# Performance work log

Measured on AMD Instinct MI355X. Metric: run time of the kernel, lower is better.

Reference implementation:

```python
import jax, jax.numpy as jnp
import numpy as np

E = 8       # num experts
T = 1024    # num tokens
H = 1024    # hidden dim
I = 1024    # intermediate dim (per gate/up half)


def setup_inputs() -> dict:
    key = jax.random.key(0)
    k1, k2, k3, k4 = jax.random.split(key, 4)
    return {
        "hidden_states": jax.random.normal(k1, (T, H), jnp.float32),
        "router_logits": jax.random.normal(k2, (T, E), jnp.float32),
        # W13 stored pre-transposed as in the module: [E, H, 2*I]
        "W13": jax.random.normal(k3, (E, H, 2 * I), jnp.float32) * 0.02,
        # W2 stored pre-transposed: [E, I, H]
        "W2": jax.random.normal(k4, (E, I, H), jnp.float32) * 0.02,
        "top_k": 2,
    }


def reference(hidden_states, router_logits, W13, W2, top_k):
    num_experts = router_logits.shape[-1]
    # --- routing: topk_softmax (softmax over all experts, then top-k) ---
    probs = jax.nn.softmax(router_logits, axis=-1)            # [T, E]
    w, idx = jax.lax.top_k(probs, top_k)                      # [T, K]
    # renormalize=True path of moe_gather
    w = w / jnp.sum(w, axis=-1, keepdims=True)
    # combine weights per expert: [T, E]
    combine = jnp.sum(jax.nn.one_hot(idx, num_experts, dtype=w.dtype) * w[..., None], axis=1)
    # --- grouped gate-up GEMM + silu_and_mul ---
    h13 = jnp.einsum('th,ehf->tef', hidden_states, W13)       # [T, E, 2I]
    gate, up = jnp.split(h13, 2, axis=-1)                     # each [T, E, I]
    act = jax.nn.silu(gate) * up                              # silu_and_mul
    # --- grouped down GEMM ---
    down = jnp.einsum('tei,eih->teh', act, W2)                # [T, E, H]
    # --- combine (moe_gather) ---
    return jnp.einsum('te,teh->th', combine, down)            # [T, H]
```

## Files before the change

kernel.cpp:

```cpp
#include <hip/hip_runtime.h>
#include <hip/hip_bf16.h>
#include <stdint.h>

#define NE    8
#define NTOK  1024
#define NH    1024
#define NI    1024
#define N13   2048
#define NPAIR 2048

typedef __attribute__((ext_vector_type(8))) short short8;
typedef __attribute__((ext_vector_type(4))) float f32x4;
typedef unsigned short u16;
typedef unsigned int   u32;

__device__ __forceinline__ u16 f2bf(float x) {
    union { float f; u32 u; } v; v.f = x;
    return (u16)((v.u + 0x7fffu + ((v.u >> 16) & 1u)) >> 16);
}

__device__ __forceinline__ void async_ld16(u16* lds, const u16* g) {
    __builtin_amdgcn_global_load_lds(
        (const __attribute__((address_space(1))) u32*)g,
        (__attribute__((address_space(3))) u32*)lds, 16, 0, 0);
}

__global__ __launch_bounds__(256) void prep_kernel(
    const float* __restrict__ logits, const float* __restrict__ X,
    int* __restrict__ counts, int* __restrict__ pair_tok,
    float* __restrict__ pair_w, u16* __restrict__ Xb)
{
    const int tid = threadIdx.x;
    if (blockIdx.x > 0) {
        const int i = (blockIdx.x - 1) * 256 + tid;
        const float4* s = (const float4*)X;
        const float4 a = s[2 * i], b = s[2 * i + 1];
        uint4 o;
        o.x = f2bf(a.x) | ((u32)f2bf(a.y) << 16);
        o.y = f2bf(a.z) | ((u32)f2bf(a.w) << 16);
        o.z = f2bf(b.x) | ((u32)f2bf(b.y) << 16);
        o.w = f2bf(b.z) | ((u32)f2bf(b.w) << 16);
        *(uint4*)(Xb + (size_t)i * 8) = o;
        return;
    }

    __shared__ int s_cnt[NE];
    __shared__ int s_base[NE];
    if (tid < NE) s_cnt[tid] = 0;
    __syncthreads();

    int eA[4][2]; int slotA[4][2]; float wA[4][2];

    #pragma unroll
    for (int i = 0; i < 4; i++) {
        const int t = tid * 4 + i;
        float l[NE];
        #pragma unroll
        for (int e = 0; e < NE; e++) l[e] = logits[t * NE + e];
        int i0 = 0;
        #pragma unroll
        for (int e = 1; e < NE; e++) if (l[e] > l[i0]) i0 = e;
        int i1 = -1;
        #pragma unroll
        for (int e = 0; e < NE; e++) {
            if (e == i0) continue;
            if (i1 < 0 || l[e] > l[i1]) i1 = e;
        }
        const float e10 = __expf(l[i1] - l[i0]);
        const float inv = 1.0f / (1.0f + e10);
        eA[i][0] = i0; eA[i][1] = i1;
        wA[i][0] = inv; wA[i][1] = e10 * inv;
        slotA[i][0] = atomicAdd(&s_cnt[i0], 1);
        slotA[i][1] = atomicAdd(&s_cnt[i1], 1);
    }
    __syncthreads();
    if (tid == 0) {
        int acc = 0;
        #pragma unroll
        for (int e = 0; e < NE; e++) { s_base[e] = acc; acc += s_cnt[e]; }
    }
    __syncthreads();
    if (tid < NE) counts[tid] = s_cnt[tid];
    #pragma unroll
    for (int i = 0; i < 4; i++) {
        const int t = tid * 4 + i;
        #pragma unroll
        for (int k = 0; k < 2; k++) {
            const int p = s_base[eA[i][k]] + slotA[i][k];
            pair_tok[p] = t;
            pair_w[p]   = wA[i][k];
        }
    }
}

__global__ __launch_bounds__(256) void cvt_w_kernel(
    const float* __restrict__ W13, u16* __restrict__ W13t,
    const float* __restrict__ W2, u16* __restrict__ W2t)
{
    __shared__ float Ts[64][65];
    const float* src; u16* dst; int K, N, bid;
    if (blockIdx.x < NE * 16 * 32) { src = W13; dst = W13t; K = NH; N = N13; bid = blockIdx.x; }
    else                           { src = W2;  dst = W2t;  K = NI; N = NH;  bid = blockIdx.x - NE * 16 * 32; }

    const int ktiles = K >> 6, ntiles = N >> 6;
    const int tpe = ktiles * ntiles;
    const int e = bid / tpe;
    const int rem = bid - e * tpe;
    const int kt = rem / ntiles, nt = rem - (rem / ntiles) * ntiles;
    const float* sb = src + ((size_t)e * K + (size_t)kt * 64) * N + nt * 64;
    const int tid = threadIdx.x;

    #pragma unroll
    for (int i = 0; i < 4; i++) {
        const int idx = tid + i * 256;
        const int r = idx >> 4, c = (idx & 15) << 2;
        const float4 v = *(const float4*)(sb + (size_t)r * N + c);
        Ts[r][c + 0] = v.x; Ts[r][c + 1] = v.y;
        Ts[r][c + 2] = v.z; Ts[r][c + 3] = v.w;
    }
    __syncthreads();
    u16* db = dst + ((size_t)e * N + (size_t)nt * 64) * K + kt * 64;
    #pragma unroll
    for (int i = 0; i < 2; i++) {
        const int u = tid + i * 256;
        const int n = u >> 3, k8 = (u & 7) << 3;
        uint4 o;
        o.x = f2bf(Ts[k8 + 0][n]) | ((u32)f2bf(Ts[k8 + 1][n]) << 16);
        o.y = f2bf(Ts[k8 + 2][n]) | ((u32)f2bf(Ts[k8 + 3][n]) << 16);
        o.z = f2bf(Ts[k8 + 4][n]) | ((u32)f2bf(Ts[k8 + 5][n]) << 16);
        o.w = f2bf(Ts[k8 + 6][n]) | ((u32)f2bf(Ts[k8 + 7][n]) << 16);
        *(uint4*)(db + (size_t)n * K + k8) = o;
    }
}

__device__ __forceinline__ bool find_tile(
    const int* __restrict__ counts, int tile, int bm, int ntn,
    int& e_o, int& mt_o, int& nt_o, int& cnt_o, int& base_o)
{
    int base = 0;
    #pragma unroll
    for (int e = 0; e < NE; e++) {
        const int cnt = counts[e];
        const int mtiles = (cnt + bm - 1) / bm;
        const int tiles = mtiles * ntn;
        if (tile < tiles) {
            e_o = e; mt_o = tile / ntn; nt_o = tile - (tile / ntn) * ntn;
            cnt_o = cnt; base_o = base; return true;
        }
        tile -= tiles; base += cnt;
    }
    return false;
}

__global__ __launch_bounds__(256) void gemm1_kernel(
    const u16* __restrict__ Xb, const u16* __restrict__ W13t,
    const int* __restrict__ counts, const int* __restrict__ pair_tok,
    u16* __restrict__ act)
{
    int e, mt, nt, cnt, base;
    if (!find_tile(counts, blockIdx.x, 128, NI / 32, e, mt, nt, cnt, base)) return;

    __shared__ u16 As[2][128 * 32];
    __shared__ u16 Bs[2][64 * 32];

    const int tid = threadIdx.x;
    const int ct  = nt * 32;

    const int m0 = tid >> 2;
    const int sw16 = (((tid & 3) ^ (m0 & 3)) << 3);
    const int t0 = pair_tok[base + min(mt * 128 + m0, cnt - 1)];
    const int t1 = pair_tok[base + min(mt * 128 + 64 + m0, cnt - 1)];
    const u16* ga0 = Xb + (size_t)t0 * NH + sw16;
    const u16* ga1 = Xb + (size_t)t1 * NH + sw16;
    const int wcol = (m0 < 32) ? (ct + m0) : (NI + ct + m0 - 32);
    const u16* gb = W13t + ((size_t)e * N13 + wcol) * 1024 + sw16;

    const int lane = tid & 63, w = tid >> 6;
    const int quad = lane >> 4, lid = lane & 15;
    const int rw = w >> 1, cw = w & 1;
    const int fsw = (quad ^ (lid & 3)) << 3;
    int aoff[4];
    #pragma unroll
    for (int mi = 0; mi < 4; mi++)
        aoff[mi] = (rw * 64 + mi * 16 + lid) * 32 + fsw;
    const int bgoff = (cw * 16 + lid) * 32 + fsw;
    const int buoff = (32 + cw * 16 + lid) * 32 + fsw;

    f32x4 accg[4] = {};
    f32x4 accu[4] = {};

#define ISSUE1(b, k0)                                        \
    {                                                        \
        async_ld16(&As[b][tid * 8],         ga0 + (k0));     \
        async_ld16(&As[b][(tid + 256) * 8], ga1 + (k0));     \
        async_ld16(&Bs[b][tid * 8],         gb  + (k0));     \
    }
#define COMP1(b)                                                               \
    {                                                                          \
        short8 av[4];                                                          \
        _Pragma("unroll") for (int mi = 0; mi < 4; mi++)                       \
            av[mi] = *(const short8*)&As[b][aoff[mi]];                         \
        const short8 gv = *(const short8*)&Bs[b][bgoff];                       \
        const short8 uv = *(const short8*)&Bs[b][buoff];                       \
        _Pragma("unroll") for (int mi = 0; mi < 4; mi++) {                     \
            accg[mi] = __builtin_amdgcn_mfma_f32_16x16x32_bf16(                \
                av[mi], gv, accg[mi], 0, 0, 0);                                \
            accu[mi] = __builtin_amdgcn_mfma_f32_16x16x32_bf16(                \
                av[mi], uv, accu[mi], 0, 0, 0);                                \
        }                                                                      \
    }

    ISSUE1(0, 0);
    int buf = 0;
    for (int k0 = 32; k0 < NH; k0 += 32) {
        __syncthreads();
        ISSUE1(buf ^ 1, k0);
        COMP1(buf);
        buf ^= 1;
    }
    __syncthreads();
    COMP1(buf);

    const int col = ct + cw * 16 + lid;
    #pragma unroll
    for (int mi = 0; mi < 4; mi++) {
        #pragma unroll
        for (int r = 0; r < 4; r++) {
            const int row = mt * 128 + rw * 64 + mi * 16 + quad * 4 + r;
            if (row < cnt) {
                const float g = accg[mi][r], u = accu[mi][r];
                const float s = g / (1.0f + __expf(-g)) * u;
                act[(size_t)(base + row) * NI + col] = f2bf(s);
            }
        }
    }
#undef ISSUE1
#undef COMP1
}

__global__ __launch_bounds__(256) void gemm2_kernel(
    const u16* __restrict__ act, const u16* __restrict__ W2t,
    const int* __restrict__ counts, const int* __restrict__ pair_tok,
    const float* __restrict__ pair_w, float* __restrict__ out)
{
    int e, mt, nt, cnt, base;
    if (!find_tile(counts, blockIdx.x, 64, NH / 64, e, mt, nt, cnt, base)) return;

    __shared__ u16 As[2][64 * 32];
    __shared__ u16 Bs[2][64 * 32];

    const int tid = threadIdx.x;
    const int ct  = nt * 64;

    const int m0 = tid >> 2;
    const int sw16 = (((tid & 3) ^ (m0 & 3)) << 3);
    const int p0 = base + min(mt * 64 + m0, cnt - 1);
    const u16* ga = act + (size_t)p0 * NI + sw16;
    const u16* gb = W2t + ((size_t)e * 1024 + ct + m0) * 1024 + sw16;

    const int lane = tid & 63, w = tid >> 6;
    const int quad = lane >> 4, lid = lane & 15;
    const int rw = w >> 1, cw = w & 1;
    const int fsw = (quad ^ (lid & 3)) << 3;
    int aoff[2], boff[2];
    #pragma unroll
    for (int mi = 0; mi < 2; mi++)
        aoff[mi] = (rw * 32 + mi * 16 + lid) * 32 + fsw;
    #pragma unroll
    for (int nj = 0; nj < 2; nj++)
        boff[nj] = (cw * 32 + nj * 16 + lid) * 32 + fsw;

    f32x4 acc[2][2] = {};

#define ISSUE2(b, k0)                                        \
    {                                                        \
        async_ld16(&As[b][tid * 8], ga + (k0));              \
        async_ld16(&Bs[b][tid * 8], gb + (k0));              \
    }
#define COMP2(b)                                                               \
    {                                                                          \
        short8 av[2], bv[2];                                                   \
        _Pragma("unroll") for (int mi = 0; mi < 2; mi++)                       \
            av[mi] = *(const short8*)&As[b][aoff[mi]];                         \
        _Pragma("unroll") for (int nj = 0; nj < 2; nj++)                       \
            bv[nj] = *(const short8*)&Bs[b][boff[nj]];                         \
        _Pragma("unroll") for (int mi = 0; mi < 2; mi++)                       \
            _Pragma("unroll") for (int nj = 0; nj < 2; nj++)                   \
                acc[mi][nj] = __builtin_amdgcn_mfma_f32_16x16x32_bf16(         \
                    av[mi], bv[nj], acc[mi][nj], 0, 0, 0);                     \
    }

    ISSUE2(0, 0);
    int buf = 0;
    for (int k0 = 32; k0 < NI; k0 += 32) {
        __syncthreads();
        ISSUE2(buf ^ 1, k0);
        COMP2(buf);
        buf ^= 1;
    }
    __syncthreads();
    COMP2(buf);

    #pragma unroll
    for (int mi = 0; mi < 2; mi++) {
        #pragma unroll
        for (int r = 0; r < 4; r++) {
            const int row = mt * 64 + rw * 32 + mi * 16 + quad * 4 + r;
            if (row < cnt) {
                const int p = base + row;
                const int t = pair_tok[p];
                const float wgt = pair_w[p];
                #pragma unroll
                for (int nj = 0; nj < 2; nj++) {
                    const int col = ct + cw * 32 + nj * 16 + lid;
                    atomicAdd(out + (size_t)t * NH + col, wgt * acc[mi][nj][r]);
                }
            }
        }
    }
#undef ISSUE2
#undef COMP2
}

extern "C" void kernel_launch(void* const* d_in, const int* in_sizes, int n_in,
                              void* d_out, int out_size, void* d_ws, size_t ws_size,
                              hipStream_t stream)
{
    const float* X      = (const float*)d_in[0];
    const float* logits = (const float*)d_in[1];
    const float* W13    = (const float*)d_in[2];
    const float* W2     = (const float*)d_in[3];
    float* out = (float*)d_out;

    char* ws = (char*)d_ws;
    int*   counts   = (int*)(ws + 0);
    int*   pair_tok = (int*)(ws + 256);
    float* pair_w   = (float*)(ws + 256 + 8192);
    u16*   Xb       = (u16*)(ws + 65536);
    u16*   W13t     = (u16*)(ws + 4194304);
    u16*   W2t      = (u16*)(ws + 4194304 + 33554432);
    u16*   act      = (u16*)(ws + 54525952);

    hipMemsetAsync(d_out, 0, (size_t)NTOK * NH * sizeof(float), stream);
    prep_kernel<<<513, 256, 0, stream>>>(logits, X, counts, pair_tok, pair_w, Xb);
    cvt_w_kernel<<<NE * 16 * 32 + NE * 16 * 16, 256, 0, stream>>>(W13, W13t, W2, W2t);

    const int grid1 = (NPAIR / 128 + NE - 1) * (NI / 32);
    const int grid2 = (NPAIR / 64 + NE - 1) * (NH / 64);
    gemm1_kernel<<<grid1, 256, 0, stream>>>(Xb, W13t, counts, pair_tok, act);
    gemm2_kernel<<<grid2, 256, 0, stream>>>(act, W2t, counts, pair_tok, pair_w, out);
}
```

Measured before the change: 190.2 us.

## Fuse MoE pipeline into one persistent cooperative kernel with grid syncs

Replaces the memset plus four separate launches (prep, weight convert, gemm1, gemm2) with one cooperative persistent kernel. It loops over work items in three phases separated by grid.sync, and the output zeroing moves into phase 0. The aim is to remove launch overhead and inter-kernel gaps, with a fallback multi-kernel path kept in case the cooperative launch fails. The cost is grid-wide barrier overhead, and the persistent grid size is capped by occupancy, which may reduce parallelism in the conversion phase.

```diff
diff --git a/kernel.cpp b/kernel.cpp
--- a/kernel.cpp
+++ b/kernel.cpp
@@ -1,6 +1,9 @@
 #include <hip/hip_runtime.h>
+#include <hip/hip_cooperative_groups.h>
 #include <hip/hip_bf16.h>
 #include <stdint.h>
+
+namespace cg = cooperative_groups;
 
 #define NE    8
 #define NTOK  1024
@@ -9,6 +12,10 @@
 #define N13   2048
 #define NPAIR 2048
 
+#define P0_ITEMS 7169
+#define G1MAX    736
+#define G2MAX    624
+
 typedef __attribute__((ext_vector_type(8))) short short8;
 typedef __attribute__((ext_vector_type(4))) float f32x4;
 typedef unsigned short u16;
@@ -23,114 +30,6 @@
     __builtin_amdgcn_global_load_lds(
         (const __attribute__((address_space(1))) u32*)g,
         (__attribute__((address_space(3))) u32*)lds, 16, 0, 0);
-}
-
-__global__ __launch_bounds__(256) void prep_kernel(
-    const float* __restrict__ logits, const float* __restrict__ X,
-    int* __restrict__ counts, int* __restrict__ pair_tok,
-    float* __restrict__ pair_w, u16* __restrict__ Xb)
-{
-    const int tid = threadIdx.x;
-    if (blockIdx.x > 0) {
-        const int i = (blockIdx.x - 1) * 256 + tid;
-        const float4* s = (const float4*)X;
-        const float4 a = s[2 * i], b = s[2 * i + 1];
-        uint4 o;
-        o.x = f2bf(a.x) | ((u32)f2bf(a.y) << 16);
-        o.y = f2bf(a.z) | ((u32)f2bf(a.w) << 16);
-        o.z = f2bf(b.x) | ((u32)f2bf(b.y) << 16);
-        o.w = f2bf(b.z) | ((u32)f2bf(b.w) << 16);
-        *(uint4*)(Xb + (size_t)i * 8) = o;
-        return;
-    }
-
-    __shared__ int s_cnt[NE];
-    __shared__ int s_base[NE];
-    if (tid < NE) s_cnt[tid] = 0;
-    __syncthreads();
-
-    int eA[4][2]; int slotA[4][2]; float wA[4][2];
-
-    #pragma unroll
-    for (int i = 0; i < 4; i++) {
-        const int t = tid * 4 + i;
-        float l[NE];
-        #pragma unroll
-        for (int e = 0; e < NE; e++) l[e] = logits[t * NE + e];
-        int i0 = 0;
-        #pragma unroll
-        for (int e = 1; e < NE; e++) if (l[e] > l[i0]) i0 = e;
-        int i1 = -1;
-        #pragma unroll
-        for (int e = 0; e < NE; e++) {
-            if (e == i0) continue;
-            if (i1 < 0 || l[e] > l[i1]) i1 = e;
-        }
-        const float e10 = __expf(l[i1] - l[i0]);
-        const float inv = 1.0f / (1.0f + e10);
-        eA[i][0] = i0; eA[i][1] = i1;
-        wA[i][0] = inv; wA[i][1] = e10 * inv;
-        slotA[i][0] = atomicAdd(&s_cnt[i0], 1);
-        slotA[i][1] = atomicAdd(&s_cnt[i1], 1);
-    }
-    __syncthreads();
-    if (tid == 0) {
-        int acc = 0;
-        #pragma unroll
-        for (int e = 0; e < NE; e++) { s_base[e] = acc; acc += s_cnt[e]; }
-    }
-    __syncthreads();
-    if (tid < NE) counts[tid] = s_cnt[tid];
-    #pragma unroll
-    for (int i = 0; i < 4; i++) {
-        const int t = tid * 4 + i;
-        #pragma unroll
-        for (int k = 0; k < 2; k++) {
-            const int p = s_base[eA[i][k]] + slotA[i][k];
-            pair_tok[p] = t;
-            pair_w[p]   = wA[i][k];
-        }
-    }
-}
-
-__global__ __launch_bounds__(256) void cvt_w_kernel(
-    const float* __restrict__ W13, u16* __restrict__ W13t,
-    const float* __restrict__ W2, u16* __restrict__ W2t)
-{
-    __shared__ float Ts[64][65];
-    const float* src; u16* dst; int K, N, bid;
-    if (blockIdx.x < NE * 16 * 32) { src = W13; dst = W13t; K = NH; N = N13; bid = blockIdx.x; }
-    else                           { src = W2;  dst = W2t;  K = NI; N = NH;  bid = blockIdx.x - NE * 16 * 32; }
-
-    const int ktiles = K >> 6, ntiles = N >> 6;
-    const int tpe = ktiles * ntiles;
-    const int e = bid / tpe;
-    const int rem = bid - e * tpe;
-    const int kt = rem / ntiles, nt = rem - (rem / ntiles) * ntiles;
-    const float* sb = src + ((size_t)e * K + (size_t)kt * 64) * N + nt * 64;
-    const int tid = threadIdx.x;
-
-    #pragma unroll
-    for (int i = 0; i < 4; i++) {
-        const int idx = tid + i * 256;
-        const int r = idx >> 4, c = (idx & 15) << 2;
-        const float4 v = *(const float4*)(sb + (size_t)r * N + c);
-        Ts[r][c + 0] = v.x; Ts[r][c + 1] = v.y;
-        Ts[r][c + 2] = v.z; Ts[r][c + 3] = v.w;
-    }
-    __syncthreads();
-    u16* db = dst + ((size_t)e * N + (size_t)nt * 64) * K + kt * 64;
-    #pragma unroll
-    for (int i = 0; i < 2; i++) {
-        const int u = tid + i * 256;
-        const int n = u >> 3, k8 = (u & 7) << 3;
-        uint4 o;
-        o.x = f2bf(Ts[k8 + 0][n]) | ((u32)f2bf(Ts[k8 + 1][n]) << 16);
-        o.y = f2bf(Ts[k8 + 2][n]) | ((u32)f2bf(Ts[k8 + 3][n]) << 16);
-        o.z = f2bf(Ts[k8 + 4][n]) | ((u32)f2bf(Ts[k8 + 5][n]) << 16);
-        o.w = f2bf(Ts[k8 + 6][n]) | ((u32)f2bf(Ts[k8 + 7][n]) << 16);
-        *(uint4*)(db + (size_t)n * K + k8) = o;
-    }
 }
 
 __device__ __forceinline__ bool find_tile(
@@ -152,17 +51,124 @@
     return false;
 }
 
-__global__ __launch_bounds__(256) void gemm1_kernel(
+__device__ __forceinline__ void phase0_item(
+    int b, char* smem,
+    const float* __restrict__ X, const float* __restrict__ logits,
+    const float* __restrict__ W13, const float* __restrict__ W2,
+    float* __restrict__ out, int* __restrict__ counts,
+    int* __restrict__ pair_tok, float* __restrict__ pair_w,
+    u16* __restrict__ Xb, u16* __restrict__ W13t, u16* __restrict__ W2t)
+{
+    const int tid = threadIdx.x;
+    if (b == 0) {
+        int* s_cnt  = (int*)smem;
+        int* s_base = s_cnt + NE;
+        if (tid < NE) s_cnt[tid] = 0;
+        __syncthreads();
+        int eA[4][2]; int slotA[4][2]; float wA[4][2];
+        #pragma unroll
+        for (int i = 0; i < 4; i++) {
+            const int t = tid * 4 + i;
+            float l[NE];
+            #pragma unroll
+            for (int e = 0; e < NE; e++) l[e] = logits[t * NE + e];
+            int i0 = 0;
+            #pragma unroll
+            for (int e = 1; e < NE; e++) if (l[e] > l[i0]) i0 = e;
+            int i1 = -1;
+            #pragma unroll
+            for (int e = 0; e < NE; e++) {
+                if (e == i0) continue;
+                if (i1 < 0 || l[e] > l[i1]) i1 = e;
+            }
+            const float e10 = __expf(l[i1] - l[i0]);
+            const float inv = 1.0f / (1.0f + e10);
+            eA[i][0] = i0; eA[i][1] = i1;
+            wA[i][0] = inv; wA[i][1] = e10 * inv;
+            slotA[i][0] = atomicAdd(&s_cnt[i0], 1);
+            slotA[i][1] = atomicAdd(&s_cnt[i1], 1);
+        }
+        __syncthreads();
+        if (tid == 0) {
+            int acc = 0;
+            #pragma unroll
+            for (int e = 0; e < NE; e++) { s_base[e] = acc; acc += s_cnt[e]; }
+        }
+        __syncthreads();
+        if (tid < NE) counts[tid] = s_cnt[tid];
+        #pragma unroll
+        for (int i = 0; i < 4; i++) {
+            const int t = tid * 4 + i;
+            #pragma unroll
+            for (int k = 0; k < 2; k++) {
+                const int p = s_base[eA[i][k]] + slotA[i][k];
+                pair_tok[p] = t;
+                pair_w[p]   = wA[i][k];
+            }
+        }
+    } else if (b <= 512) {
+        const int i = (b - 1) * 256 + tid;
+        const float4* s = (const float4*)X;
+        const float4 a = s[2 * i], c = s[2 * i + 1];
+        uint4 o;
+        o.x = f2bf(a.x) | ((u32)f2bf(a.y) << 16);
+        o.y = f2bf(a.z) | ((u32)f2bf(a.w) << 16);
+        o.z = f2bf(c.x) | ((u32)f2bf(c.y) << 16);
+        o.w = f2bf(c.z) | ((u32)f2bf(c.w) << 16);
+        *(uint4*)(Xb + (size_t)i * 8) = o;
+    } else if (b <= 1024) {
+        const int i = ((b - 513) * 256 + tid) * 8;
+        const float4 z = make_float4(0.f, 0.f, 0.f, 0.f);
+        *(float4*)(out + i)     = z;
+        *(float4*)(out + i + 4) = z;
+    } else {
+        float (*Ts)[65] = (float(*)[65])smem;
+        const int wb = b - 1025;
+        const float* src; u16* dst; int K, N, tb;
+        if (wb < 4096) { src = W13; dst = W13t; K = NH; N = N13; tb = wb; }
+        else           { src = W2;  dst = W2t;  K = NI; N = NH;  tb = wb - 4096; }
+        const int ktiles = K >> 6, ntiles = N >> 6;
+        const int tpe = ktiles * ntiles;
+        const int e = tb / tpe;
+        const int rem = tb - e * tpe;
+        const int kt = rem / ntiles, nt = rem - (rem / ntiles) * ntiles;
+        const float* sb = src + ((size_t)e * K + (size_t)kt * 64) * N + nt * 64;
+        #pragma unroll
+        for (int i = 0; i < 4; i++) {
+            const int idx = tid + i * 256;
+            const int r = idx >> 4, c = (idx & 15) << 2;
+            const float4 v = *(const float4*)(sb + (size_t)r * N + c);
+            Ts[r][c + 0] = v.x; Ts[r][c + 1] = v.y;
+            Ts[r][c + 2] = v.z; Ts[r][c + 3] = v.w;
+        }
+        __syncthreads();
+        u16* db = dst + ((size_t)e * N + (size_t)nt * 64) * K + kt * 64;
+        #pragma unroll
+        for (int i = 0; i < 2; i++) {
+            const int u = tid + i * 256;
+            const int n = u >> 3, k8 = (u & 7) << 3;
+            uint4 o;
+            o.x = f2bf(Ts[k8 + 0][n]) | ((u32)f2bf(Ts[k8 + 1][n]) << 16);
+            o.y = f2bf(Ts[k8 + 2][n]) | ((u32)f2bf(Ts[k8 + 3][n]) << 16);
+            o.z = f2bf(Ts[k8 + 4][n]) | ((u32)f2bf(Ts[k8 + 5][n]) << 16);
+            o.w = f2bf(Ts[k8 + 6][n]) | ((u32)f2bf(Ts[k8 + 7][n]) << 16);
+            *(uint4*)(db + (size_t)n * K + k8) = o;
+        }
+    }
+}
+
+__device__ __forceinline__ void gemm1_tile(
+    int tile, char* smem,
     const u16* __restrict__ Xb, const u16* __restrict__ W13t,
     const int* __restrict__ counts, const int* __restrict__ pair_tok,
     u16* __restrict__ act)
 {
+    __syncthreads();
     int e, mt, nt, cnt, base;
-    if (!find_tile(counts, blockIdx.x, 128, NI / 32, e, mt, nt, cnt, base)) return;
-
-    __shared__ u16 As[2][128 * 32];
-    __shared__ u16 Bs[2][64 * 32];
-
+    if (!find_tile(counts, tile, 128, NI / 32, e, mt, nt, cnt, base)) return;
+
+    u16* As = (u16*)smem;
+    u16* Bs = (u16*)(smem + 16384);
     const int tid = threadIdx.x;
     const int ct  = nt * 32;
 
@@ -189,19 +195,19 @@
     f32x4 accg[4] = {};
     f32x4 accu[4] = {};
 
-#define ISSUE1(b, k0)                                        \
-    {                                                        \
-        async_ld16(&As[b][tid * 8],         ga0 + (k0));     \
-        async_ld16(&As[b][(tid + 256) * 8], ga1 + (k0));     \
-        async_ld16(&Bs[b][tid * 8],         gb  + (k0));     \
+#define ISSUE1(b, k0)                                             \
+    {                                                             \
+        async_ld16(&As[(b) * 4096 + tid * 8],         ga0 + (k0));\
+        async_ld16(&As[(b) * 4096 + (tid + 256) * 8], ga1 + (k0));\
+        async_ld16(&Bs[(b) * 2048 + tid * 8],         gb  + (k0));\
     }
 #define COMP1(b)                                                               \
     {                                                                          \
         short8 av[4];                                                          \
         _Pragma("unroll") for (int mi = 0; mi < 4; mi++)                       \
-            av[mi] = *(const short8*)&As[b][aoff[mi]];                         \
-        const short8 gv = *(const short8*)&Bs[b][bgoff];                       \
-        const short8 uv = *(const short8*)&Bs[b][buoff];                       \
+            av[mi] = *(const short8*)&As[(b) * 4096 + aoff[mi]];               \
+        const short8 gv = *(const short8*)&Bs[(b) * 2048 + bgoff];             \
+        const short8 uv = *(const short8*)&Bs[(b) * 2048 + buoff];             \
         _Pragma("unroll") for (int mi = 0; mi < 4; mi++) {                     \
             accg[mi] = __builtin_amdgcn_mfma_f32_16x16x32_bf16(                \
                 av[mi], gv, accg[mi], 0, 0, 0);                                \
@@ -238,17 +244,18 @@
 #undef COMP1
 }
 
-__global__ __launch_bounds__(256) void gemm2_kernel(
+__device__ __forceinline__ void gemm2_tile(
+    int tile, char* smem,
     const u16* __restrict__ act, const u16* __restrict__ W2t,
     const int* __restrict__ counts, const int* __restrict__ pair_tok,
     const float* __restrict__ pair_w, float* __restrict__ out)
 {
+    __syncthreads();
     int e, mt, nt, cnt, base;
-    if (!find_tile(counts, blockIdx.x, 64, NH / 64, e, mt, nt, cnt, base)) return;
-
-    __shared__ u16 As[2][64 * 32];
-    __shared__ u16 Bs[2][64 * 32];
-
+    if (!find_tile(counts, tile, 64, NH / 64, e, mt, nt, cnt, base)) return;
+
+    u16* As = (u16*)smem;
+    u16* Bs = (u16*)(smem + 8192);
     const int tid = threadIdx.x;
     const int ct  = nt * 64;
 
@@ -272,18 +279,18 @@
 
     f32x4 acc[2][2] = {};
 
-#define ISSUE2(b, k0)                                        \
-    {                                                        \
-        async_ld16(&As[b][tid * 8], ga + (k0));              \
-        async_ld16(&Bs[b][tid * 8], gb + (k0));              \
+#define ISSUE2(b, k0)                                      \
+    {                                                      \
+        async_ld16(&As[(b) * 2048 + tid * 8], ga + (k0));  \
+        async_ld16(&Bs[(b) * 2048 + tid * 8], gb + (k0));  \
     }
 #define COMP2(b)                                                               \
     {                                                                          \
         short8 av[2], bv[2];                                                   \
         _Pragma("unroll") for (int mi = 0; mi < 2; mi++)                       \
-            av[mi] = *(const short8*)&As[b][aoff[mi]];                         \
+            av[mi] = *(const short8*)&As[(b) * 2048 + aoff[mi]];               \
         _Pragma("unroll") for (int nj = 0; nj < 2; nj++)                       \
-            bv[nj] = *(const short8*)&Bs[b][boff[nj]];                         \
+            bv[nj] = *(const short8*)&Bs[(b) * 2048 + boff[nj]];               \
         _Pragma("unroll") for (int mi = 0; mi < 2; mi++)                       \
             _Pragma("unroll") for (int nj = 0; nj < 2; nj++)                   \
                 acc[mi][nj] = __builtin_amdgcn_mfma_f32_16x16x32_bf16(         \
@@ -322,6 +329,57 @@
 #undef COMP2
 }
 
+__global__ __launch_bounds__(256, 2) void moe_coop(
+    const float* X, const float* logits, const float* W13, const float* W2,
+    float* out, int* counts, int* pair_tok, float* pair_w,
+    u16* Xb, u16* W13t, u16* W2t, u16* act)
+{
+    __shared__ __align__(16) char smem[24576];
+    cg::grid_group grid = cg::this_grid();
+
+    for (int b = blockIdx.x; b < P0_ITEMS; b += gridDim.x) {
+        phase0_item(b, smem, X, logits, W13, W2, out,
+                    counts, pair_tok, pair_w, Xb, W13t, W2t);
+        __syncthreads();
+    }
+    __threadfence();
+    grid.sync();
+
+    for (int t = blockIdx.x; t < G1MAX; t += gridDim.x)
+        gemm1_tile(t, smem, Xb, W13t, counts, pair_tok, act);
+    __threadfence();
+    grid.sync();
+
+    for (int t = blockIdx.x; t < G2MAX; t += gridDim.x)
+        gemm2_tile(t, smem, act, W2t, counts, pair_tok, pair_w, out);
+}
+
+__global__ __launch_bounds__(256) void prep_all_kernel(
+    const float* X, const float* logits, const float* W13, const float* W2,
+    float* out, int* counts, int* pair_tok, float* pair_w,
+    u16* Xb, u16* W13t, u16* W2t)
+{
+    __shared__ __align__(16) char smem[24576];
+    phase0_item(blockIdx.x, smem, X, logits, W13, W2, out,
+                counts, pair_tok, pair_w, Xb, W13t, W2t);
+}
+
+__global__ __launch_bounds__(256, 2) void gemm1_kernel(
+    const u16* Xb, const u16* W13t, const int* counts, const int* pair_tok,
+    u16* act)
+{
+    __shared__ __align__(16) char smem[24576];
+    gemm1_tile(blockIdx.x, smem, Xb, W13t, counts, pair_tok, act);
+}
+
+__global__ __launch_bounds__(256, 2) void gemm2_kernel(
+    const u16* act, const u16* W2t, const int* counts, const int* pair_tok,
+    const float* pair_w, float* out)
+{
+    __shared__ __align__(16) char smem[24576];
+    gemm2_tile(blockIdx.x, smem, act, W2t, counts, pair_tok, pair_w, out);
+}
+
 extern "C" void kernel_launch(void* const* d_in, const int* in_sizes, int n_in,
                               void* d_out, int out_size, void* d_ws, size_t ws_size,
                               hipStream_t stream)
@@ -341,12 +399,25 @@
     u16*   W2t      = (u16*)(ws + 4194304 + 33554432);
     u16*   act      = (u16*)(ws + 54525952);
 
-    hipMemsetAsync(d_out, 0, (size_t)NTOK * NH * sizeof(float), stream);
-    prep_kernel<<<513, 256, 0, stream>>>(logits, X, counts, pair_tok, pair_w, Xb);
-    cvt_w_kernel<<<NE * 16 * 32 + NE * 16 * 16, 256, 0, stream>>>(W13, W13t, W2, W2t);
-
-    const int grid1 = (NPAIR / 128 + NE - 1) * (NI / 32);
-    const int grid2 = (NPAIR / 64 + NE - 1) * (NH / 64);
-    gemm1_kernel<<<grid1, 256, 0, stream>>>(Xb, W13t, counts, pair_tok, act);
-    gemm2_kernel<<<grid2, 256, 0, stream>>>(act, W2t, counts, pair_tok, pair_w, out);
-}
+    hipError_t st = hipErrorUnknown;
+    int occ = 0;
+    hipError_t oe = hipOccupancyMaxActiveBlocksPerMultiprocessor(
+        &occ, (const void*)moe_coop, 256, 0);
+    if (oe == hipSuccess && occ >= 1) {
+        int grid = occ * 256;
+        if (grid > 768) grid = 768;
+        void* kargs[] = {
+            (void*)&X, (void*)&logits, (void*)&W13, (void*)&W2, (void*)&out,
+            (void*)&counts, (void*)&pair_tok, (void*)&pair_w,
+            (void*)&Xb, (void*)&W13t, (void*)&W2t, (void*)&act
+        };
+        st = hipLaunchCooperativeKernel((const void*)moe_coop, dim3(grid),
+                                        dim3(256), kargs, 0, stream);
+    }
+    if (st != hipSuccess) {
+        prep_all_kernel<<<P0_ITEMS, 256, 0, stream>>>(
+            X, logits, W13, W2, out, counts, pair_tok, pair_w, Xb, W13t, W2t);
+        gemm1_kernel<<<G1MAX, 256, 0, stream>>>(Xb, W13t, counts, pair_tok, act);
+        gemm2_kernel<<<G2MAX, 256, 0, stream>>>(act, W2t, counts, pair_tok, pair_w, out);
+    }
+}
```

Result: slower. 446.1 us (+134.6%).
